# Kernel optimization log

Measured on AMD Instinct MI355X. Metric: run time of the kernel, lower is better.

The kernel has to match this reference:

```python
import jax, jax.numpy as jnp
import numpy as np

BETA = 0.25  # commitment_cost
K = 512      # num_embeddings
D = 64       # embedding_dim


def setup_inputs() -> dict:
    key = jax.random.key(0)
    k1, k2 = jax.random.split(key)
    z = jax.random.normal(k1, (8, D, 16, 64, 64), dtype=jnp.float32)
    # torch init: uniform_(-1/K, 1/K)
    emb = jax.random.uniform(k2, (K, D), dtype=jnp.float32,
                             minval=-1.0 / K, maxval=1.0 / K)
    return {"z": z, "emb": emb}


def reference(z, emb):
    B, Dc, d, h, w = z.shape
    # (B, D, d, h, w) -> (N, D), N = B*d*h*w
    z_flat = jnp.transpose(z, (0, 2, 3, 4, 1)).reshape(-1, Dc)
    # squared euclidean distances to each codebook entry: (N, K)
    dists = (jnp.sum(z_flat * z_flat, axis=1, keepdims=True)
             - 2.0 * (z_flat @ emb.T)
             + jnp.sum(emb * emb, axis=1))
    indices = jnp.argmin(dists, axis=1)                      # (N,)
    z_q = emb[indices]                                       # (N, D) gather
    z_q = jnp.transpose(z_q.reshape(B, d, h, w, Dc), (0, 4, 1, 2, 3))
    codebook_loss = jnp.mean((z_q - jax.lax.stop_gradient(z)) ** 2)
    commitment_loss = jnp.mean((jax.lax.stop_gradient(z_q) - z) ** 2)
    loss = codebook_loss + BETA * commitment_loss
    # straight-through estimator
    z_q_st = z + jax.lax.stop_gradient(z_q - z)
    return (z_q_st, loss, indices.reshape(B, d, h, w))
```

## Files before the change

### kernel.cpp

```cpp
#include <hip/hip_runtime.h>


#define NK       512
#define DD       64
#define LOSS_OFF 33554432
#define IDX_OFF  33554433
#define EE_FOFF  4

typedef float f32x4 __attribute__((ext_vector_type(4)));
#define CONST_AS __attribute__((address_space(4)))

__device__ __forceinline__ float np_sumsq64(const float* v) {
#pragma clang fp contract(off)
    float r[8];
    #pragma unroll
    for (int j = 0; j < 8; ++j) {
        float s = v[j] * v[j];
        r[j] = s;
    }
    #pragma unroll
    for (int i = 8; i < 64; i += 8) {
        #pragma unroll
        for (int j = 0; j < 8; ++j) {
            float s = v[i + j] * v[i + j];
            r[j] += s;
        }
    }
    return ((r[0] + r[1]) + (r[2] + r[3])) + ((r[4] + r[5]) + (r[6] + r[7]));
}

__global__ void vq_ee(const float* __restrict__ emb, float* __restrict__ ws) {
    const int k = blockIdx.x * 256 + threadIdx.x;
    float row[DD];
    const float* er = emb + k * DD;
    #pragma unroll
    for (int c = 0; c < DD; ++c) row[c] = er[c];
    ws[EE_FOFF + k] = np_sumsq64(row);
}

__global__ __launch_bounds__(256)
__attribute__((amdgpu_waves_per_eu(4, 4)))
void vq_main(const float* __restrict__ z, const float* __restrict__ emb,
             float* __restrict__ out, float* __restrict__ ws) {
    const int n  = blockIdx.x * 256 + threadIdx.x;
    const int b  = n >> 16;
    const int sp = n & 65535;
    const float* zp = z + ((size_t)b << 22) + sp;

    float zr[DD];
    #pragma unroll
    for (int c = 0; c < DD; ++c) zr[c] = zp[(size_t)c << 16];
    const float zz = np_sumsq64(zr);

    const CONST_AS f32x4* e4  = (const CONST_AS f32x4*)emb;
    const CONST_AS float* eec = (const CONST_AS float*)(ws + EE_FOFF);

    float best = 3.4e38f;
    int   bi   = 0;

    #pragma unroll 1
    for (int k = 0; k < NK; ++k) {
        const CONST_AS f32x4* er = e4 + (k << 4);
        float m = 0.f;
        #pragma unroll
        for (int c4 = 0; c4 < 16; ++c4) {
            const f32x4 e = er[c4];
            m = fmaf(zr[c4 * 4 + 0], e.x, m);
            m = fmaf(zr[c4 * 4 + 1], e.y, m);
            m = fmaf(zr[c4 * 4 + 2], e.z, m);
            m = fmaf(zr[c4 * 4 + 3], e.w, m);
        }
        const float d = fmaf(-2.f, m, zz) + eec[k];
        if (d < best) { best = d; bi = k; }
    }

    float* op = out + ((size_t)b << 22) + sp;
    const float4* brow = (const float4*)(emb + bi * DD);
    float lsum = 0.f;
    #pragma unroll
    for (int c4 = 0; c4 < 16; ++c4) {
        float4 e = brow[c4];
        float eq[4] = { e.x, e.y, e.z, e.w };
        #pragma unroll
        for (int j = 0; j < 4; ++j) {
            const int c = c4 * 4 + j;
            float d = eq[j] - zr[c];
            lsum = fmaf(d, d, lsum);
            op[(size_t)c << 16] = eq[j];
        }
    }
    out[IDX_OFF + n] = (float)bi;

    #pragma unroll
    for (int off = 32; off > 0; off >>= 1) lsum += __shfl_down(lsum, off);
    if ((threadIdx.x & 63) == 0)
        atomicAdd((double*)ws, (double)lsum);
}

__global__ void vq_finalize(const float* __restrict__ ws, float* __restrict__ out) {
    out[LOSS_OFF] = (float)(((const double*)ws)[0] * (1.25 / 33554432.0));
}

extern "C" void kernel_launch(void* const* d_in, const int* in_sizes, int n_in,
                              void* d_out, int out_size, void* d_ws, size_t ws_size,
                              hipStream_t stream) {
    const float* z   = (const float*)d_in[0];
    const float* emb = (const float*)d_in[1];
    float* out = (float*)d_out;
    float* ws  = (float*)d_ws;

    hipMemsetAsync(d_ws, 0, 16, stream);
    vq_ee<<<dim3(2), dim3(256), 0, stream>>>(emb, ws);
    vq_main<<<dim3(2048), dim3(256), 0, stream>>>(z, emb, out, ws);
    vq_finalize<<<dim3(1), dim3(1), 0, stream>>>(ws, out);
}
```

Measured before the change: 760.7 us.

## Stage codebook in LDS and compute two points per thread

The codebook is now streamed through shared memory in four 128-entry chunks instead of being read through scalar constant loads. Each thread handles two positions, so every LDS read of a codebook vector feeds two FMA chains, and the grid is halved. The workspace memset is folded into the vq_ee kernel. The cost is higher register pressure (occupancy hint lowered to 3 waves/EU), extra barriers, and LDS traffic in place of scalar-cache broadcasts.

```diff
diff --git a/kernel.cpp b/kernel.cpp
--- a/kernel.cpp
+++ b/kernel.cpp
@@ -8,7 +8,6 @@
 #define EE_FOFF  4
 
 typedef float f32x4 __attribute__((ext_vector_type(4)));
-#define CONST_AS __attribute__((address_space(4)))
 
 __device__ __forceinline__ float np_sumsq64(const float* v) {
 #pragma clang fp contract(off)
@@ -31,6 +30,10 @@
 
 __global__ void vq_ee(const float* __restrict__ emb, float* __restrict__ ws) {
     const int k = blockIdx.x * 256 + threadIdx.x;
+    if (blockIdx.x == 0 && threadIdx.x == 0) {
+        ((double*)ws)[0] = 0.0;
+        ((double*)ws)[1] = 0.0;
+    }
     float row[DD];
     const float* er = emb + k * DD;
     #pragma unroll
@@ -39,61 +42,93 @@
 }
 
 __global__ __launch_bounds__(256)
-__attribute__((amdgpu_waves_per_eu(4, 4)))
+__attribute__((amdgpu_waves_per_eu(3, 3)))
 void vq_main(const float* __restrict__ z, const float* __restrict__ emb,
              float* __restrict__ out, float* __restrict__ ws) {
-    const int n  = blockIdx.x * 256 + threadIdx.x;
-    const int b  = n >> 16;
-    const int sp = n & 65535;
-    const float* zp = z + ((size_t)b << 22) + sp;
+    __shared__ f32x4 elds[2048];
+    __shared__ float eelds[NK];
 
-    float zr[DD];
+    const int tid = threadIdx.x;
+    const int n0  = blockIdx.x * 512 + tid;
+    const int n1  = n0 + 256;
+    const int b   = n0 >> 16;
+    const int sp  = n0 & 65535;
+    const float* zp0 = z + ((size_t)b << 22) + sp;
+    const float* zp1 = zp0 + 256;
+
+    eelds[tid]       = ws[EE_FOFF + tid];
+    eelds[tid + 256] = ws[EE_FOFF + tid + 256];
+
+    float za[DD], zb[DD];
     #pragma unroll
-    for (int c = 0; c < DD; ++c) zr[c] = zp[(size_t)c << 16];
-    const float zz = np_sumsq64(zr);
+    for (int c = 0; c < DD; ++c) za[c] = zp0[(size_t)c << 16];
+    #pragma unroll
+    for (int c = 0; c < DD; ++c) zb[c] = zp1[(size_t)c << 16];
+    const float zz0 = np_sumsq64(za);
+    const float zz1 = np_sumsq64(zb);
 
-    const CONST_AS f32x4* e4  = (const CONST_AS f32x4*)emb;
-    const CONST_AS float* eec = (const CONST_AS float*)(ws + EE_FOFF);
+    const f32x4* eg = (const f32x4*)emb;
 
-    float best = 3.4e38f;
-    int   bi   = 0;
+    float best0 = 3.4e38f, best1 = 3.4e38f;
+    int   bi0   = 0,        bi1   = 0;
 
     #pragma unroll 1
-    for (int k = 0; k < NK; ++k) {
-        const CONST_AS f32x4* er = e4 + (k << 4);
-        float m = 0.f;
+    for (int p = 0; p < 4; ++p) {
+        __syncthreads();
         #pragma unroll
-        for (int c4 = 0; c4 < 16; ++c4) {
-            const f32x4 e = er[c4];
-            m = fmaf(zr[c4 * 4 + 0], e.x, m);
-            m = fmaf(zr[c4 * 4 + 1], e.y, m);
-            m = fmaf(zr[c4 * 4 + 2], e.z, m);
-            m = fmaf(zr[c4 * 4 + 3], e.w, m);
+        for (int r = 0; r < 8; ++r)
+            elds[r * 256 + tid] = eg[p * 2048 + r * 256 + tid];
+        __syncthreads();
+
+        #pragma unroll 1
+        for (int kl = 0; kl < 128; ++kl) {
+            float m0 = 0.f, m1 = 0.f;
+            #pragma unroll
+            for (int c4 = 0; c4 < 16; ++c4) {
+                const f32x4 e = elds[kl * 16 + c4];
+                const int c = c4 * 4;
+                m0 = fmaf(za[c + 0], e.x, m0);  m1 = fmaf(zb[c + 0], e.x, m1);
+                m0 = fmaf(za[c + 1], e.y, m0);  m1 = fmaf(zb[c + 1], e.y, m1);
+                m0 = fmaf(za[c + 2], e.z, m0);  m1 = fmaf(zb[c + 2], e.z, m1);
+                m0 = fmaf(za[c + 3], e.w, m0);  m1 = fmaf(zb[c + 3], e.w, m1);
+            }
+            const int k = p * 128 + kl;
+            const float ee = eelds[k];
+            const float d0 = fmaf(-2.f, m0, zz0) + ee;
+            const float d1 = fmaf(-2.f, m1, zz1) + ee;
+            if (d0 < best0) { best0 = d0; bi0 = k; }
+            if (d1 < best1) { best1 = d1; bi1 = k; }
         }
-        const float d = fmaf(-2.f, m, zz) + eec[k];
-        if (d < best) { best = d; bi = k; }
     }
 
-    float* op = out + ((size_t)b << 22) + sp;
-    const float4* brow = (const float4*)(emb + bi * DD);
+    float* op0 = out + ((size_t)b << 22) + sp;
+    float* op1 = op0 + 256;
+    const float4* br0 = (const float4*)(emb + bi0 * DD);
+    const float4* br1 = (const float4*)(emb + bi1 * DD);
     float lsum = 0.f;
     #pragma unroll
     for (int c4 = 0; c4 < 16; ++c4) {
-        float4 e = brow[c4];
-        float eq[4] = { e.x, e.y, e.z, e.w };
+        float4 e0 = br0[c4];
+        float4 e1 = br1[c4];
+        float eq0[4] = { e0.x, e0.y, e0.z, e0.w };
+        float eq1[4] = { e1.x, e1.y, e1.z, e1.w };
         #pragma unroll
         for (int j = 0; j < 4; ++j) {
             const int c = c4 * 4 + j;
-            float d = eq[j] - zr[c];
-            lsum = fmaf(d, d, lsum);
-            op[(size_t)c << 16] = eq[j];
+            float da = eq0[j] - za[c];
+            float db = eq1[j] - zb[c];
+            lsum = fmaf(da, da, lsum);
+            lsum = fmaf(db, db, lsum);
+            op0[(size_t)c << 16] = eq0[j];
+            op1[(size_t)c << 16] = eq1[j];
         }
     }
-    out[IDX_OFF + n] = (float)bi;
+    out[IDX_OFF + n0] = (float)bi0;
+    out[IDX_OFF + n1] = (float)bi1;
 
     #pragma unroll
     for (int off = 32; off > 0; off >>= 1) lsum += __shfl_down(lsum, off);
-    if ((threadIdx.x & 63) == 0)
+    if ((tid & 63) == 0)
         atomicAdd((double*)ws, (double)lsum);
 }
 
@@ -109,8 +144,7 @@
     float* out = (float*)d_out;
     float* ws  = (float*)d_ws;
 
-    hipMemsetAsync(d_ws, 0, 16, stream);
     vq_ee<<<dim3(2), dim3(256), 0, stream>>>(emb, ws);
-    vq_main<<<dim3(2048), dim3(256), 0, stream>>>(z, emb, out, ws);
+    vq_main<<<dim3(1024), dim3(256), 0, stream>>>(z, emb, out, ws);
     vq_finalize<<<dim3(1), dim3(1), 0, stream>>>(ws, out);
 }
```

Result: faster. 730.3 us (-4.0%).
